# Kernel optimization log

Measured on AMD Instinct MI355X. Metric: run time of the kernel, lower is better.

The kernel has to match this reference:

```python
import jax, jax.numpy as jnp
import numpy as np


def setup_inputs() -> dict:
    key = jax.random.key(0)
    k1, k2, k3, k4, k5, k6 = jax.random.split(key, 6)
    B, N, T, F = 16, 256, 64, 128  # batch, num_hnodes==in_dim==out_dim, time_win, feat
    x = jax.random.normal(k1, (B, N, T, F), dtype=jnp.float32)
    entryid = jax.random.randint(k2, (B, N, T), 0, N, dtype=jnp.int64)
    jobid = jax.random.randint(k3, (B, N, T), 0, 8, dtype=jnp.int64)
    rackid = jax.random.randint(k4, (B, N, T), 0, 16, dtype=jnp.int64)
    full_weight = jax.random.normal(k5, (N, N), dtype=jnp.float32) * 0.05
    bias = jax.random.normal(k6, (N,), dtype=jnp.float32) * 0.01
    gamma = jnp.ones((N,), dtype=jnp.float32)
    beta = jnp.zeros((N,), dtype=jnp.float32)
    return {"x": x, "entryid": entryid, "jobid": jobid, "rackid": rackid,
            "full_weight": full_weight, "bias": bias, "gamma": gamma, "beta": beta}


def reference(x, entryid, jobid, rackid, full_weight, bias, gamma, beta):
    # NOTE: in the original torch module the LayerNorm output is overwritten
    # (y = x.permute(...)) and MaskLinear never adds its bias; we reproduce
    # that exact math, so norm/bias are dead w.r.t. the output.
    B, N, T, F = x.shape  # N == in_dim == out_dim == num_hnodes, T == time_win
    out_features = full_weight.shape[0]

    inp = jnp.transpose(x, (0, 2, 3, 1))  # [B, T, F, N]

    # gather per-(batch,node,time) weight columns: [out, B, N, T]
    weight = full_weight[:, entryid.reshape(-1)].reshape(out_features, B, N, T)

    # job-equality mask: [B, N, N, T] -> permuted to [N, B, N, T]
    same_job = (jobid[:, :, None, :] == jobid[:, None, :, :]) \
               & (jobid[:, :, None, :] != 0) & (jobid[:, None, :, :] != 0)
    mask = jnp.transpose(same_job, (1, 0, 2, 3)).astype(x.dtype)

    masked_weight = weight * mask  # [out(=N), B, N, T] via broadcast over dim0

    # einsum 'bijk,lbki->bijl' with i=T, j=F, k=N, l=out
    y = jnp.einsum('bijk,lbki->bijl', inp, masked_weight)
    y = jax.nn.relu(y)            # dropout is identity at eval
    y = jnp.transpose(y, (0, 3, 1, 2))  # [B, out, T, F]
    return x + y
```

## Files before the change

kernel.cpp:

```cpp
#include <hip/hip_runtime.h>
#include <stdint.h>

typedef float  f32x4 __attribute__((ext_vector_type(4)));
typedef short  s16x8 __attribute__((ext_vector_type(8)));
typedef short  s16x4 __attribute__((ext_vector_type(4)));
typedef unsigned int uint32;

#define B_ 16
#define N_ 256
#define T_ 64
#define F_ 128
#define KT 32
#define NT 8

#define BLKSTR 544
#define X_TILE_STR (16 * BLKSTR)
#define X_OFF 0
#define W_OFF (NT * X_TILE_STR)
#define E_OFF (W_OFF + 32 * BLKSTR)
#define J_OFF (E_OFF + N_ * 4)
#define LDS_SZ (J_OFF + N_)

#define TRREAD(dst, addr) \
  asm volatile("ds_read_b64_tr_b16 %0, %1" : "=v"(dst) : "v"(addr))

#define LGKM_FENCE() asm volatile("s_waitcnt lgkmcnt(0)" ::: "memory")
#define BAR()                                    \
  do {                                           \
    LGKM_FENCE();                                \
    __builtin_amdgcn_s_barrier();                \
    asm volatile("" ::: "memory");               \
  } while (0)

__device__ __forceinline__ unsigned short f2bf(float f) {
  union { float f; unsigned int u; } v; v.f = f;
  unsigned int u = v.u;
  return (unsigned short)((u + 0x7fffu + ((u >> 16) & 1u)) >> 16);
}
__device__ __forceinline__ float bf2f(unsigned short h) {
  union { unsigned int u; float f; } v; v.u = ((unsigned int)h) << 16;
  return v.f;
}

__global__ void wtrans_kernel(const float* __restrict__ fw,
                              unsigned short* __restrict__ fwTb) {
  int c = blockIdx.x;
  int l = threadIdx.x;
  fwTb[c * N_ + l] = f2bf(fw[l * N_ + c]);
}

__global__ __launch_bounds__(512, 2) void fused_kernel(
    const float* __restrict__ x,
    const int* __restrict__ entry,
    const int* __restrict__ job,
    const unsigned short* __restrict__ fwTb,
    float* __restrict__ out) {
  __shared__ __align__(16) char smem[LDS_SZ];
  const uint32 lds_u = (uint32)(uintptr_t)(&smem[0]);

  const int tid = threadIdx.x;
  const int bid = blockIdx.x;
  const int b = bid >> 6;
  const int t = bid & 63;

  if (tid < N_) {
    int idx = (b * N_ + tid) * T_ + t;
    *(int*)(smem + E_OFF + 4 * tid) = entry[idx];
    smem[J_OFF + tid] = (char)job[idx];
  }

  const int xk  = tid >> 4;
  const int xf0 = (tid & 15) << 3;

  {
    const float* src = x + ((b * N_ + xk) * T_ + t) * F_ + xf0;
    f32x4 r0 = *(const f32x4*)(src);
    f32x4 r1 = *(const f32x4*)(src + 4);
    s16x8 pk;
#pragma unroll
    for (int i = 0; i < 4; ++i) {
      pk[i]     = (short)f2bf(r0[i]);
      pk[i + 4] = (short)f2bf(r1[i]);
    }
    char* dst = smem + X_OFF +
                (((xk >> 4) * 8 + (xf0 >> 4)) * BLKSTR) +
                ((xk & 15) * 32) + ((xf0 & 15) * 2);
    *(s16x8*)dst = pk;
  }
  BAR();

  const int lane = tid & 63;
  const int wid  = tid >> 6;
  const int wl   = wid & 3;
  const int wf   = wid >> 2;

  f32x4 acc[4][4];
#pragma unroll
  for (int i = 0; i < 4; ++i)
#pragma unroll
    for (int j = 0; j < 4; ++j) acc[i][j] = (f32x4){0.f, 0.f, 0.f, 0.f};

  for (int kt = 0; kt < NT; ++kt) {
    {
      const int wk  = tid & 31;
      const int wlg = tid >> 5;
      const int k   = kt * KT + wk;
      const int ev  = *(const int*)(smem + E_OFF + 4 * k);
      const unsigned char jk = (unsigned char)smem[J_OFF + k];
      const unsigned short* wrow = fwTb + ev * N_;
      const uint32 kin = (uint32)((wk & 15) * 32);
      const int kb = (wk >> 4) & 1;
#pragma unroll
      for (int it = 0; it < 2; ++it) {
        const int l0 = wlg * 16 + it * 8;
        s16x8 wv = *(const s16x8*)(wrow + l0);
        uint64_t jl8 = *(const uint64_t*)(smem + J_OFF + l0);
        s16x8 m;
#pragma unroll
        for (int i = 0; i < 8; ++i) {
          unsigned char jl = (unsigned char)(jl8 >> (8 * i));
          m[i] = (jk != 0 && jl == jk) ? wv[i] : (short)0;
        }
        char* dst = smem + W_OFF + ((kb * 16 + wlg) * BLKSTR) + kin + it * 16;
        *(s16x8*)dst = m;
      }
    }

    f32x4 p0, p1;
    if (kt + 1 < NT) {
      const float* src = x + ((b * N_ + (kt + 1) * KT + xk) * T_ + t) * F_ + xf0;
      p0 = *(const f32x4*)(src);
      p1 = *(const f32x4*)(src + 4);
    }

    BAR();

    {
      s16x4 ah[4][2], bh[4][2];
      const uint32 wbase = lds_u + W_OFF + (uint32)(lane * 8);
      const uint32 xbase = lds_u + X_OFF + (uint32)(kt * X_TILE_STR + lane * 8);
#pragma unroll
      for (int li = 0; li < 4; ++li) {
        const uint32 a0 = wbase + (uint32)(((0 * 16) + (wl * 4 + li)) * BLKSTR);
        const uint32 a1 = wbase + (uint32)(((1 * 16) + (wl * 4 + li)) * BLKSTR);
        TRREAD(ah[li][0], a0);
        TRREAD(ah[li][1], a1);
      }
#pragma unroll
      for (int fi = 0; fi < 4; ++fi) {
        const uint32 b0 = xbase + (uint32)(((0 * 8) + (wf * 4 + fi)) * BLKSTR);
        const uint32 b1 = xbase + (uint32)(((1 * 8) + (wf * 4 + fi)) * BLKSTR);
        TRREAD(bh[fi][0], b0);
        TRREAD(bh[fi][1], b1);
      }
      LGKM_FENCE();
      __builtin_amdgcn_sched_barrier(0);
#pragma unroll
      for (int li = 0; li < 4; ++li) {
        s16x8 af = __builtin_shufflevector(ah[li][0], ah[li][1],
                                           0, 1, 2, 3, 4, 5, 6, 7);
#pragma unroll
        for (int fi = 0; fi < 4; ++fi) {
          s16x8 bf = __builtin_shufflevector(bh[fi][0], bh[fi][1],
                                             0, 1, 2, 3, 4, 5, 6, 7);
          acc[li][fi] =
              __builtin_amdgcn_mfma_f32_16x16x32_bf16(af, bf, acc[li][fi], 0, 0, 0);
        }
      }
    }

    if (kt + 1 < NT) {
      s16x8 pk;
#pragma unroll
      for (int i = 0; i < 4; ++i) {
        pk[i]     = (short)f2bf(p0[i]);
        pk[i + 4] = (short)f2bf(p1[i]);
      }
      char* dst = smem + X_OFF + (kt + 1) * X_TILE_STR +
                  (((xk >> 4) * 8 + (xf0 >> 4)) * BLKSTR) +
                  ((xk & 15) * 32) + ((xf0 & 15) * 2);
      *(s16x8*)dst = pk;
    }

    BAR();
  }

  const int g4   = (lane >> 4) * 4;
  const int fcol = lane & 15;
#pragma unroll
  for (int li = 0; li < 4; ++li) {
    const int Lb = wl * 4 + li;
    const uint32 rb = lds_u + X_OFF + (uint32)((Lb >> 1) * X_TILE_STR +
                       ((Lb & 1) * 8) * BLKSTR + lane * 8);
    s16x4 xr[4];
#pragma unroll
    for (int fi = 0; fi < 4; ++fi) {
      TRREAD(xr[fi], rb + (uint32)((wf * 4 + fi) * BLKSTR));
    }
    LGKM_FENCE();
    __builtin_amdgcn_sched_barrier(0);
    const int l0 = Lb * 16 + g4;
#pragma unroll
    for (int fi = 0; fi < 4; ++fi) {
      const int f = (wf * 4 + fi) * 16 + fcol;
      float* op = out + ((b * N_ + l0) * T_ + t) * F_ + f;
#pragma unroll
      for (int r = 0; r < 4; ++r) {
        float y = acc[li][fi][r];
        y = y > 0.f ? y : 0.f;
        op[r * (T_ * F_)] = bf2f((unsigned short)xr[fi][r]) + y;
      }
    }
  }
}

extern "C" void kernel_launch(void* const* d_in, const int* in_sizes, int n_in,
                              void* d_out, int out_size, void* d_ws,
                              size_t ws_size, hipStream_t stream) {
  (void)in_sizes; (void)n_in; (void)out_size; (void)ws_size;
  const float* x     = (const float*)d_in[0];
  const int*   entry = (const int*)d_in[1];
  const int*   job   = (const int*)d_in[2];
  const float* fw    = (const float*)d_in[4];
  unsigned short* fwTb = (unsigned short*)d_ws;

  hipLaunchKernelGGL(wtrans_kernel, dim3(N_), dim3(N_), 0, stream, fw, fwTb);
  hipLaunchKernelGGL(fused_kernel, dim3(B_ * T_), dim3(512), 0, stream,
                     x, entry, job, (const unsigned short*)fwTb, (float*)d_out);
}
```

Measured before the change: 76.68 us.

## Prefetch all x tiles upfront and double-buffer masked weight tiles

Issues all eight x tile loads at kernel start and converts them into LDS in one pass, so the global x loads are no longer serialized with the k-loop. The masked weight tile now lives in a double buffer: the next tile's weight row is fetched from global before the MFMAs and written to the other buffer afterwards, which cuts the loop from two barriers per iteration to one. It also hoists the job-id row reads out of the loop. The cost is more registers for the upfront loads and a larger LDS footprint, which could lower occupancy below the two blocks per CU the launch bounds ask for.

New measurement: 76.88 us. About the same (+0.3%).

```diff
diff --git a/kernel.cpp b/kernel.cpp
--- a/kernel.cpp
+++ b/kernel.cpp
@@ -17,7 +17,8 @@
 #define X_TILE_STR (16 * BLKSTR)
 #define X_OFF 0
 #define W_OFF (NT * X_TILE_STR)
-#define E_OFF (W_OFF + 32 * BLKSTR)
+#define W_BUF_STR (32 * BLKSTR)
+#define E_OFF (W_OFF + 2 * W_BUF_STR)
 #define J_OFF (E_OFF + N_ * 4)
 #define LDS_SZ (J_OFF + N_)
 
@@ -63,29 +64,70 @@
   const int b = bid >> 6;
   const int t = bid & 63;
 
+  int e_val = 0, j_val = 0;
   if (tid < N_) {
-    int idx = (b * N_ + tid) * T_ + t;
-    *(int*)(smem + E_OFF + 4 * tid) = entry[idx];
-    smem[J_OFF + tid] = (char)job[idx];
+    const int idx = (b * N_ + tid) * T_ + t;
+    e_val = entry[idx];
+    j_val = job[idx];
   }
 
   const int xk  = tid >> 4;
   const int xf0 = (tid & 15) << 3;
-
+  const float* xsrc = x + ((b * N_ + xk) * T_ + t) * F_ + xf0;
+#define XLD(i)                                                            \
+  f32x4 q##i##a = *(const f32x4*)(xsrc + (i) * (KT * T_ * F_));           \
+  f32x4 q##i##b = *(const f32x4*)(xsrc + (i) * (KT * T_ * F_) + 4);
+  XLD(0) XLD(1) XLD(2) XLD(3) XLD(4) XLD(5) XLD(6) XLD(7)
+#undef XLD
+
+  if (tid < N_) {
+    *(int*)(smem + E_OFF + 4 * tid) = e_val;
+    smem[J_OFF + tid] = (char)j_val;
+  }
+  BAR();
+
+  const int wk  = tid & 31;
+  const int wlg = tid >> 5;
+  s16x8 gv0, gv1;
+  unsigned char gjk;
   {
-    const float* src = x + ((b * N_ + xk) * T_ + t) * F_ + xf0;
-    f32x4 r0 = *(const f32x4*)(src);
-    f32x4 r1 = *(const f32x4*)(src + 4);
-    s16x8 pk;
-#pragma unroll
-    for (int i = 0; i < 4; ++i) {
-      pk[i]     = (short)f2bf(r0[i]);
-      pk[i + 4] = (short)f2bf(r1[i]);
-    }
-    char* dst = smem + X_OFF +
-                (((xk >> 4) * 8 + (xf0 >> 4)) * BLKSTR) +
-                ((xk & 15) * 32) + ((xf0 & 15) * 2);
-    *(s16x8*)dst = pk;
+    const int ev = *(const int*)(smem + E_OFF + 4 * wk);
+    gjk = (unsigned char)smem[J_OFF + wk];
+    const unsigned short* wrow = fwTb + ev * N_ + wlg * 16;
+    gv0 = *(const s16x8*)(wrow);
+    gv1 = *(const s16x8*)(wrow + 8);
+  }
+
+  const uint64_t jl80 = *(const uint64_t*)(smem + J_OFF + wlg * 16);
+  const uint64_t jl81 = *(const uint64_t*)(smem + J_OFF + wlg * 16 + 8);
+
+  const uint32 xdst_in = (uint32)((((xk >> 4) * 8 + (xf0 >> 4)) * BLKSTR) +
+                                  ((xk & 15) * 32) + ((xf0 & 15) * 2));
+#define XST(i)                                                            \
+  {                                                                       \
+    s16x8 pk;                                                             \
+    _Pragma("unroll") for (int _j = 0; _j < 4; ++_j) {                    \
+      pk[_j]     = (short)f2bf(q##i##a[_j]);                              \
+      pk[_j + 4] = (short)f2bf(q##i##b[_j]);                              \
+    }                                                                     \
+    *(s16x8*)(smem + X_OFF + (i) * X_TILE_STR + xdst_in) = pk;            \
+  }
+  XST(0) XST(1) XST(2) XST(3) XST(4) XST(5) XST(6) XST(7)
+#undef XST
+
+  const uint32 wwr_base =
+      (uint32)(((wk >> 4) * 16 + wlg) * BLKSTR + (wk & 15) * 32);
+  {
+    s16x8 m0, m1;
+#pragma unroll
+    for (int i = 0; i < 8; ++i) {
+      const unsigned char a0 = (unsigned char)(jl80 >> (8 * i));
+      const unsigned char a1 = (unsigned char)(jl81 >> (8 * i));
+      m0[i] = (gjk != 0 && a0 == gjk) ? gv0[i] : (short)0;
+      m1[i] = (gjk != 0 && a1 == gjk) ? gv1[i] : (short)0;
+    }
+    *(s16x8*)(smem + W_OFF + wwr_base) = m0;
+    *(s16x8*)(smem + W_OFF + wwr_base + 16) = m1;
   }
   BAR();
 
@@ -101,57 +143,32 @@
     for (int j = 0; j < 4; ++j) acc[i][j] = (f32x4){0.f, 0.f, 0.f, 0.f};
 
   for (int kt = 0; kt < NT; ++kt) {
-    {
-      const int wk  = tid & 31;
-      const int wlg = tid >> 5;
-      const int k   = kt * KT + wk;
-      const int ev  = *(const int*)(smem + E_OFF + 4 * k);
-      const unsigned char jk = (unsigned char)smem[J_OFF + k];
-      const unsigned short* wrow = fwTb + ev * N_;
-      const uint32 kin = (uint32)((wk & 15) * 32);
-      const int kb = (wk >> 4) & 1;
-#pragma unroll
-      for (int it = 0; it < 2; ++it) {
-        const int l0 = wlg * 16 + it * 8;
-        s16x8 wv = *(const s16x8*)(wrow + l0);
-        uint64_t jl8 = *(const uint64_t*)(smem + J_OFF + l0);
-        s16x8 m;
-#pragma unroll
-        for (int i = 0; i < 8; ++i) {
-          unsigned char jl = (unsigned char)(jl8 >> (8 * i));
-          m[i] = (jk != 0 && jl == jk) ? wv[i] : (short)0;
-        }
-        char* dst = smem + W_OFF + ((kb * 16 + wlg) * BLKSTR) + kin + it * 16;
-        *(s16x8*)dst = m;
-      }
-    }
-
-    f32x4 p0, p1;
+    s16x8 pv0, pv1;
+    unsigned char pjk = 0;
     if (kt + 1 < NT) {
-      const float* src = x + ((b * N_ + (kt + 1) * KT + xk) * T_ + t) * F_ + xf0;
-      p0 = *(const f32x4*)(src);
-      p1 = *(const f32x4*)(src + 4);
-    }
-
-    BAR();
+      const int k = (kt + 1) * KT + wk;
+      const int ev = *(const int*)(smem + E_OFF + 4 * k);
+      pjk = (unsigned char)smem[J_OFF + k];
+      const unsigned short* wrow = fwTb + ev * N_ + wlg * 16;
+      pv0 = *(const s16x8*)(wrow);
+      pv1 = *(const s16x8*)(wrow + 8);
+    }
 
     {
       s16x4 ah[4][2], bh[4][2];
-      const uint32 wbase = lds_u + W_OFF + (uint32)(lane * 8);
-      const uint32 xbase = lds_u + X_OFF + (uint32)(kt * X_TILE_STR + lane * 8);
+      const uint32 wbase =
+          lds_u + W_OFF + (uint32)((kt & 1) * W_BUF_STR) + (uint32)(lane * 8);
+      const uint32 xbase =
+          lds_u + X_OFF + (uint32)(kt * X_TILE_STR) + (uint32)(lane * 8);
 #pragma unroll
       for (int li = 0; li < 4; ++li) {
-        const uint32 a0 = wbase + (uint32)(((0 * 16) + (wl * 4 + li)) * BLKSTR);
-        const uint32 a1 = wbase + (uint32)(((1 * 16) + (wl * 4 + li)) * BLKSTR);
-        TRREAD(ah[li][0], a0);
-        TRREAD(ah[li][1], a1);
+        TRREAD(ah[li][0], wbase + (uint32)((wl * 4 + li) * BLKSTR));
+        TRREAD(ah[li][1], wbase + (uint32)((16 + wl * 4 + li) * BLKSTR));
       }
 #pragma unroll
       for (int fi = 0; fi < 4; ++fi) {
-        const uint32 b0 = xbase + (uint32)(((0 * 8) + (wf * 4 + fi)) * BLKSTR);
-        const uint32 b1 = xbase + (uint32)(((1 * 8) + (wf * 4 + fi)) * BLKSTR);
-        TRREAD(bh[fi][0], b0);
-        TRREAD(bh[fi][1], b1);
+        TRREAD(bh[fi][0], xbase + (uint32)((wf * 4 + fi) * BLKSTR));
+        TRREAD(bh[fi][1], xbase + (uint32)((8 + wf * 4 + fi) * BLKSTR));
       }
       LGKM_FENCE();
       __builtin_amdgcn_sched_barrier(0);
@@ -167,22 +184,23 @@
               __builtin_amdgcn_mfma_f32_16x16x32_bf16(af, bf, acc[li][fi], 0, 0, 0);
         }
       }
+      __builtin_amdgcn_sched_barrier(0);
     }
 
     if (kt + 1 < NT) {
-      s16x8 pk;
-#pragma unroll
-      for (int i = 0; i < 4; ++i) {
-        pk[i]     = (short)f2bf(p0[i]);
-        pk[i + 4] = (short)f2bf(p1[i]);
-      }
-      char* dst = smem + X_OFF + (kt + 1) * X_TILE_STR +
-                  (((xk >> 4) * 8 + (xf0 >> 4)) * BLKSTR) +
-                  ((xk & 15) * 32) + ((xf0 & 15) * 2);
-      *(s16x8*)dst = pk;
-    }
-
-    BAR();
+      s16x8 m0, m1;
+#pragma unroll
+      for (int i = 0; i < 8; ++i) {
+        const unsigned char a0 = (unsigned char)(jl80 >> (8 * i));
+        const unsigned char a1 = (unsigned char)(jl81 >> (8 * i));
+        m0[i] = (pjk != 0 && a0 == pjk) ? pv0[i] : (short)0;
+        m1[i] = (pjk != 0 && a1 == pjk) ? pv1[i] : (short)0;
+      }
+      char* wb = smem + W_OFF + ((kt + 1) & 1) * W_BUF_STR + wwr_base;
+      *(s16x8*)(wb) = m0;
+      *(s16x8*)(wb + 16) = m1;
+      BAR();
+    }
   }
 
   const int g4   = (lane >> 4) * 4;
```
